# Kernel tuning notes

Hardware: AMD Instinct MI355X
Metric: run time of the kernel (lower is better)

Reference implementation:

```python
import jax, jax.numpy as jnp
import numpy as np

T = 32768       # sequence length (batch=1 in original forward)
DY = 63         # mark dim; input_size = DY + 1 = 64
D_IN = 64
H = 256         # hidden_size
OUT = 32        # out_size
NI = 1024       # number of inducing points


def _lstm_scan(x, w_ih, w_hh, b_ih, b_hh, reverse):
    """Single-direction LSTM over [T, D] input, batch=1. PyTorch gate order i,f,g,o."""
    xg = x @ w_ih.T + (b_ih + b_hh)  # [T, 4H], input projection precomputed

    def step(carry, xg_t):
        h, c = carry
        g = xg_t + h @ w_hh.T
        i, f, gg, o = jnp.split(g, 4)
        c = jax.nn.sigmoid(f) * c + jax.nn.sigmoid(i) * jnp.tanh(gg)
        h = jax.nn.sigmoid(o) * jnp.tanh(c)
        return (h, c), h

    init = (jnp.zeros((H,), x.dtype), jnp.zeros((H,), x.dtype))
    _, hs = jax.lax.scan(step, init, xg, reverse=reverse)
    return hs  # [T, H]


def _bilstm(x, layer_params):
    for (wf, uf, bif, bhf, wb, ub, bib, bhb) in layer_params:
        hf = _lstm_scan(x, wf, uf, bif, bhf, False)
        hb = _lstm_scan(x, wb, ub, bib, bhb, True)
        x = jnp.concatenate([hf, hb], axis=-1)  # [T, 2H]
    return x


def setup_inputs() -> dict:
    key = jax.random.key(0)
    ks = iter(jax.random.split(key, 24))
    s = 1.0 / np.sqrt(H)  # PyTorch LSTM uniform(-1/sqrt(H), 1/sqrt(H)) init
    def U(shape):
        return jax.random.uniform(next(ks), shape, jnp.float32, -s, s)
    inp = {
        "Y": jax.random.normal(next(ks), (T, DY), jnp.float32),
        "dT": jax.random.uniform(next(ks), (T,), jnp.float32),
        "induce_idx": jnp.sort(jax.random.randint(next(ks), (NI,), 0, T)),
        # layer 0: input D_IN; layer 1: input 2H (bidirectional)
        "w_ih_l0f": U((4 * H, D_IN)), "w_hh_l0f": U((4 * H, H)), "b_ih_l0f": U((4 * H,)), "b_hh_l0f": U((4 * H,)),
        "w_ih_l0b": U((4 * H, D_IN)), "w_hh_l0b": U((4 * H, H)), "b_ih_l0b": U((4 * H,)), "b_hh_l0b": U((4 * H,)),
        "w_ih_l1f": U((4 * H, 2 * H)), "w_hh_l1f": U((4 * H, H)), "b_ih_l1f": U((4 * H,)), "b_hh_l1f": U((4 * H,)),
        "w_ih_l1b": U((4 * H, 2 * H)), "w_hh_l1b": U((4 * H, H)), "b_ih_l1b": U((4 * H,)), "b_hh_l1b": U((4 * H,)),
        "fc_weight": jax.random.normal(next(ks), (2 * H, 2 * OUT), jnp.float32),
    }
    return inp


def reference(Y, dT, induce_idx,
              w_ih_l0f, w_hh_l0f, b_ih_l0f, b_hh_l0f,
              w_ih_l0b, w_hh_l0b, b_ih_l0b, b_hh_l0b,
              w_ih_l1f, w_hh_l1f, b_ih_l1f, b_hh_l1f,
              w_ih_l1b, w_hh_l1b, b_ih_l1b, b_hh_l1b,
              fc_weight):
    x = jnp.concatenate([Y, dT[:, None]], axis=1)  # [T, D_IN]
    layer_params = [
        (w_ih_l0f, w_hh_l0f, b_ih_l0f, b_hh_l0f, w_ih_l0b, w_hh_l0b, b_ih_l0b, b_hh_l0b),
        (w_ih_l1f, w_hh_l1f, b_ih_l1f, b_hh_l1f, w_ih_l1b, w_hh_l1b, b_ih_l1b, b_hh_l1b),
    ]
    h = _bilstm(x, layer_params)          # [T, 2H]
    out = h @ fc_weight                    # [T, 2*OUT]
    sel = out[induce_idx]                  # [NI, 2*OUT]
    return sel[:, :OUT], sel[:, OUT:]
```

## Files before the change

### kernel.cpp

```cpp
#include <hip/hip_runtime.h>

typedef unsigned int u32;
typedef unsigned short u16;
typedef _Float16 f16;
typedef _Float16 f16x2 __attribute__((ext_vector_type(2)));
typedef _Float16 f16x4 __attribute__((ext_vector_type(4)));

#define T_SEQ 32768

static const size_t OFF_DT   = 0;
static const size_t OFF_FLG  = 1024;
static const size_t OFF_MAP  = 4096;
static const size_t OFF_H1G  = 135168;
static const size_t OFF_BIAS = 1183744;
static const size_t OFF_FCW  = 1200128;
static const size_t OFF_WQ8  = 1331200;
static const size_t OFF_WIH0 = 3428352;
static const size_t OFF_WIH1 = 3690496;
static const size_t OFF_XQ   = 5787648;
static const size_t OFF_H0   = 9981952;
static const size_t OFF_XG   = 43536384;
static const size_t XG_DIR   = (size_t)T_SEQ * 1024 * 2;
static const size_t NEED_PAR = OFF_XG + 2 * XG_DIR;

__device__ __forceinline__ float bf2f(u16 u) {
  union { u32 i; float f; } v; v.i = ((u32)u) << 16; return v.f;
}
__device__ __forceinline__ u16 f2bf(float f) {
  union { float f; u32 i; } v; v.f = f;
  u32 u = v.i;
  return (u16)((u + 0x7fffu + ((u >> 16) & 1u)) >> 16);
}
__device__ __forceinline__ u32 packf2(float a, float b) {
  f16x2 p; p.x = (f16)a; p.y = (f16)b;
  return __builtin_bit_cast(u32, p);
}
__device__ __forceinline__ u32 bf2f2(u32 v) {
  union { u32 i; float f; } lo, hi;
  lo.i = v << 16; hi.i = v & 0xffff0000u;
  return packf2(lo.f, hi.f);
}
__device__ __forceinline__ float ldf(const void* p, size_t i, u32 isf) {
  return isf ? ((const float*)p)[i] : bf2f(((const u16*)p)[i]);
}
__device__ __forceinline__ float fdot2f(f16x2 a, f16x2 b, float c) {
#if __has_builtin(__builtin_amdgcn_fdot2)
  return __builtin_amdgcn_fdot2(a, b, c, false);
#else
  return c + (float)a.x * (float)b.x + (float)a.y * (float)b.y;
#endif
}
__device__ __forceinline__ float fdotu(u32 a, u32 b, float c) {
  return fdot2f(__builtin_bit_cast(f16x2, a), __builtin_bit_cast(f16x2, b), c);
}
__device__ __forceinline__ int sdot4(u32 a, u32 b, int c) {
#if __has_builtin(__builtin_amdgcn_sdot4)
  return __builtin_amdgcn_sdot4((int)a, (int)b, c, false);
#else
  int r = c;
#pragma unroll
  for (int j = 0; j < 4; ++j)
    r += (int)(signed char)(a >> (8 * j)) * (int)(signed char)(b >> (8 * j));
  return r;
#endif
}
__device__ __forceinline__ int dpp_xor1(int x) {
#if __has_builtin(__builtin_amdgcn_update_dpp)
  return __builtin_amdgcn_update_dpp(0, x, 0xB1, 0xF, 0xF, true);
#else
  return __shfl_xor(x, 1);
#endif
}
__device__ __forceinline__ int dpp_xor2(int x) {
#if __has_builtin(__builtin_amdgcn_update_dpp)
  return __builtin_amdgcn_update_dpp(0, x, 0x4E, 0xF, 0xF, true);
#else
  return __shfl_xor(x, 2);
#endif
}
__device__ __forceinline__ int dpp_ror8(int x) {
#if __has_builtin(__builtin_amdgcn_update_dpp)
  return __builtin_amdgcn_update_dpp(0, x, 0x128, 0xF, 0xF, true);
#else
  return __shfl_xor(x, 8);
#endif
}
__device__ __forceinline__ int swz_xor4(int x) {
#if __has_builtin(__builtin_amdgcn_ds_swizzle)
  return __builtin_amdgcn_ds_swizzle(x, 0x101F);
#else
  return __shfl_xor(x, 4);
#endif
}
template <int CTRL>
__device__ __forceinline__ float dpp_bcastf(float x) {
#if __has_builtin(__builtin_amdgcn_update_dpp)
  return __builtin_bit_cast(float,
      __builtin_amdgcn_update_dpp(0, __builtin_bit_cast(int, x), CTRL, 0xF, 0xF, true));
#else
  return __shfl(x, (threadIdx.x & ~3) + (CTRL & 3));
#endif
}
__device__ __forceinline__ float tanhf_fast(float x) {
  return 1.0f - 2.0f * __builtin_amdgcn_rcpf(1.0f + __builtin_amdgcn_exp2f(2.8853900817779268f * x));
}
__device__ __forceinline__ void wg_barrier_lds() {
  asm volatile("s_waitcnt lgkmcnt(0)" ::: "memory");
  __builtin_amdgcn_s_barrier();
  asm volatile("" ::: "memory");
}

__global__ void k_detect(const u16* __restrict__ probe, u32* __restrict__ dt) {
  __shared__ int cnt;
  if (threadIdx.x == 0) cnt = 0;
  __syncthreads();
  int bad = 0;
  for (int i = threadIdx.x; i < 8192; i += 256) {
    float v = bf2f(probe[i]);
    if (!(v * v <= 16.0f)) bad++;
  }
  atomicAdd(&cnt, bad);
  __syncthreads();
  if (threadIdx.x == 0) *dt = (cnt > 64) ? 1u : 0u;
}

__global__ void k_conv_pairs(const void* __restrict__ src, u32* __restrict__ dst,
                             int np, const u32* __restrict__ dtp) {
  u32 isf = *dtp;
  int i = blockIdx.x * 256 + threadIdx.x;
  if (i >= np) return;
  if (isf) {
    const float* s = (const float*)src;
    dst[i] = packf2(s[2 * i], s[2 * i + 1]);
  } else {
    dst[i] = bf2f2(((const u32*)src)[i]);
  }
}

__global__ void k_quant(const void* __restrict__ src, u32* __restrict__ dst,
                        const u32* __restrict__ dtp) {
  u32 isf = *dtp;
  int i = blockIdx.x * 256 + threadIdx.x;
  int row = i >> 6, c = i & 63;
  u32 out = 0;
#pragma unroll
  for (int j = 0; j < 4; ++j) {
    float w = ldf(src, (size_t)row * 256 + 4 * c + j, isf);
    int q = (int)rintf(w * 2048.0f);
    q = q > 127 ? 127 : (q < -127 ? -127 : q);
    out |= ((u32)(q & 0xff)) << (8 * j);
  }
  dst[i] = out;
}

__global__ void k_conv_misc(const void* bi0f, const void* bh0f, const void* bi0b, const void* bh0b,
                            const void* bi1f, const void* bh1f, const void* bi1b, const void* bh1b,
                            const void* fcb, float* __restrict__ bias, float* __restrict__ fcw,
                            u32* __restrict__ flags, int* __restrict__ map,
                            const u32* __restrict__ dtp) {
  u32 isf = *dtp;
  int i = blockIdx.x * 256 + threadIdx.x;
  if (i < 4096) {
    int ld = i >> 10, r = i & 1023;
    const void* bi; const void* bh;
    if (ld == 0)      { bi = bi0f; bh = bh0f; }
    else if (ld == 1) { bi = bi0b; bh = bh0b; }
    else if (ld == 2) { bi = bi1f; bh = bh1f; }
    else              { bi = bi1b; bh = bh1b; }
    bias[i] = ldf(bi, r, isf) + ldf(bh, r, isf);
  } else if (i < 36864) {
    fcw[i - 4096] = ldf(fcb, i - 4096, isf);
  } else if (i < 36992) {
    flags[i - 36864] = 0;
  } else if (i < 69760) {
    map[i - 36992] = -1;
  }
}

__global__ void k_conv_x(const void* __restrict__ Y, const void* __restrict__ dT,
                         u32* __restrict__ xq, const u32* __restrict__ dtp) {
  u32 isf = *dtp;
  int i = blockIdx.x * 256 + threadIdx.x;
  if (i >= T_SEQ * 32) return;
  int t = i >> 5, m = i & 31, k2 = 2 * m;
  float a = ldf(Y, (size_t)t * 63 + k2, isf);
  float b = (k2 + 1 < 63) ? ldf(Y, (size_t)t * 63 + k2 + 1, isf) : ldf(dT, t, isf);
  xq[i] = packf2(a, b);
}

__global__ void k_map_set(const int* __restrict__ idx, int* __restrict__ map) {
  int i = blockIdx.x * 256 + threadIdx.x;
  if (i < 1024) map[idx[i]] = i;
}

__global__ __launch_bounds__(256) void k_gemm(
    const u32* __restrict__ Aq, const u32* __restrict__ Wc,
    const float* __restrict__ bias, f16* __restrict__ xgT, int Kp, int rev) {
  int t0 = blockIdx.x << 6, r0 = blockIdx.y << 6;
  int tid = threadIdx.x, tx = tid & 15, ty = tid >> 4;
  __shared__ u32 As[64][33];
  __shared__ u32 Bs[64][33];
  float acc[4][4] = {};
  for (int kp0 = 0; kp0 < Kp; kp0 += 32) {
#pragma unroll
    for (int i = 0; i < 8; ++i) {
      int idx = tid + (i << 8);
      int row = idx >> 5, kp = idx & 31, kpg = kp0 + kp;
      As[row][kp] = Aq[(size_t)(t0 + row) * Kp + kpg];
      Bs[row][kp] = Wc[(size_t)(r0 + row) * Kp + kpg];
    }
    __syncthreads();
#pragma unroll 4
    for (int kk = 0; kk < 32; ++kk) {
      u32 av[4], bv[4];
#pragma unroll
      for (int i = 0; i < 4; ++i) av[i] = As[ty * 4 + i][kk];
#pragma unroll
      for (int i = 0; i < 4; ++i) bv[i] = Bs[tx * 4 + i][kk];
#pragma unroll
      for (int i = 0; i < 4; ++i)
#pragma unroll
        for (int j = 0; j < 4; ++j)
          acc[i][j] = fdotu(av[i], bv[j], acc[i][j]);
    }
    __syncthreads();
  }
  int tb = t0 + (ty << 2);
#pragma unroll
  for (int j = 0; j < 4; ++j) {
    int rr = r0 + tx * 4 + j;
    float b = bias[rr];
    f16 v0 = (f16)(acc[0][j] + b);
    f16 v1 = (f16)(acc[1][j] + b);
    f16 v2 = (f16)(acc[2][j] + b);
    f16 v3 = (f16)(acc[3][j] + b);
    size_t base = (size_t)rr * T_SEQ;
    f16x4 v;
    size_t pos;
    if (rev) { pos = base + (size_t)(T_SEQ - 4 - tb); v = (f16x4){v3, v2, v1, v0}; }
    else     { pos = base + (size_t)tb;               v = (f16x4){v0, v1, v2, v3}; }
    *(f16x4*)(xgT + pos) = v;
  }
}

template <bool HASMAP>
__global__ __launch_bounds__(1024)
__attribute__((amdgpu_waves_per_eu(4, 4))) void k_recur2(
    const f16* __restrict__ xgT, const u32* __restrict__ wq,
    f16* __restrict__ h_full, f16* __restrict__ h1g,
    const int* __restrict__ map, int dir0) {
  const int dir = dir0 + blockIdx.x;
  const int tid = threadIdx.x;
  const int g16 = tid >> 4;
  const int s = tid & 15;
  const int u = (g16 << 2) + (s >> 2);
  const u32* wqd = wq + ((size_t)dir << 16);

  __shared__ __align__(16) unsigned char hb8[2][256];

  uint4 w[16];
  {
    const uint4* pw = (const uint4*)wqd;
#pragma unroll
    for (int t = 0; t < 16; ++t) {
      int r = t ^ s;
      w[t] = pw[(size_t)((((r & 3) << 8) + (g16 << 2) + (r >> 2)) * 16 + s)];
    }
  }

  if (tid < 128) ((u32*)hb8)[tid] = 0;

  const float ksc = 1.0f / (2048.0f * 127.0f);
  const float sk = ((s & 3) == 2) ? 2.8853900817779268f : -1.4426950408889634f;
  const float aa = ((s & 3) == 2) ? -2.0f : 1.0f;
  const float bb = ((s & 3) == 2) ? 1.0f : 0.0f;

  const f16* xg_d = xgT + (size_t)blockIdx.x * ((size_t)T_SEQ * 1024);
  const f16* xrow = xg_d + (size_t)(((s & 3) << 8) | u) * T_SEQ;

  const int tstep = dir ? -1 : 1;
  int t = dir ? (T_SEQ - 1) : 0;
  int mp = HASMAP ? map[t] : -1;
  float c_state = 0.f;

  f16* hout = h_full ? (h_full + (size_t)t * 512 + (dir << 8) + u) : nullptr;
  const ptrdiff_t hstride = (ptrdiff_t)tstep * 512;

  uint4 xcur = *(const uint4*)xrow;
  uint4 xnxt = xcur;

  __syncthreads();

  for (int ch = 0; ch < T_SEQ / 8; ++ch) {
    if (ch + 1 < T_SEQ / 8) xnxt = *(const uint4*)(xrow + (((size_t)ch + 1) << 3));
#pragma unroll
    for (int j = 0; j < 8; ++j) {
      u32 dw = (j >> 1) == 0 ? xcur.x : (j >> 1) == 1 ? xcur.y
             : (j >> 1) == 2 ? xcur.z : xcur.w;
      f16x2 pr = __builtin_bit_cast(f16x2, dw);
      float xb = (float)((j & 1) ? pr.y : pr.x);

      int ms = mp;
      if (HASMAP) {
        int tn = t + tstep;
        int idx2 = ((unsigned)tn < T_SEQ) ? tn : t;
        mp = map[idx2];
      }

      uint4 hv = ((const uint4*)hb8)[((j & 1) << 4) + s];

      int a0, a1, a2, a3, a4, a5, a6, a7, a8, a9, a10, a11, a12, a13, a14, a15;
#define DOTSLOT(A, T)                                             \
      A = sdot4(w[T].w, hv.w,                                     \
          sdot4(w[T].z, hv.z,                                     \
          sdot4(w[T].y, hv.y,                                     \
          sdot4(w[T].x, hv.x, 0))));
      DOTSLOT(a0, 0)   DOTSLOT(a1, 1)   DOTSLOT(a2, 2)   DOTSLOT(a3, 3)
      DOTSLOT(a4, 4)   DOTSLOT(a5, 5)   DOTSLOT(a6, 6)   DOTSLOT(a7, 7)
      DOTSLOT(a8, 8)   DOTSLOT(a9, 9)   DOTSLOT(a10, 10) DOTSLOT(a11, 11)
      DOTSLOT(a12, 12) DOTSLOT(a13, 13) DOTSLOT(a14, 14) DOTSLOT(a15, 15)
#undef DOTSLOT
      int b0 = a0 + dpp_xor1(a1);
      int b1 = a2 + dpp_xor1(a3);
      int b2 = a4 + dpp_xor1(a5);
      int b3 = a6 + dpp_xor1(a7);
      int b4 = a8 + dpp_xor1(a9);
      int b5 = a10 + dpp_xor1(a11);
      int b6 = a12 + dpp_xor1(a13);
      int b7 = a14 + dpp_xor1(a15);
      int c0 = b0 + dpp_xor2(b1);
      int c1 = b2 + dpp_xor2(b3);
      int c2 = b4 + dpp_xor2(b5);
      int c3 = b6 + dpp_xor2(b7);
      int d0 = c0 + swz_xor4(c1);
      int d1 = c2 + swz_xor4(c3);
      int e  = d0 + dpp_ror8(d1);

      float x = __builtin_fmaf((float)e, ksc, xb);
      float r = __builtin_amdgcn_rcpf(1.0f + __builtin_amdgcn_exp2f(sk * x));
      float g = __builtin_fmaf(aa, r, bb);
      float gi = dpp_bcastf<0x00>(g);
      float gf = dpp_bcastf<0x55>(g);
      float gg = dpp_bcastf<0xAA>(g);
      float go = dpp_bcastf<0xFF>(g);
      c_state = __builtin_fmaf(gf, c_state, gi * gg);
      float h = go * tanhf_fast(c_state);
      int q8 = (int)rintf(h * 127.0f);
      if ((s & 3) == 0) {
        hb8[(j & 1) ^ 1][u] = (unsigned char)(q8 & 0xff);
        if (h_full) *hout = (f16)h;
        if (HASMAP && ms >= 0) h1g[(size_t)ms * 512 + (dir << 8) + u] = (f16)h;
      }
      wg_barrier_lds();
      t += tstep;
      hout += hstride;
    }
    xcur = xnxt;
  }
}

__global__ void k_fc(const f16* __restrict__ hbase, const int* __restrict__ mapn,
                     const int* __restrict__ idx, const float* __restrict__ fcw,
                     void* __restrict__ out, const u32* __restrict__ dtp) {
  u32 isf = *dtp;
  int n = blockIdx.x;
  int cc = threadIdx.x;
  int slot = mapn ? mapn[idx[n]] : idx[n];
  const f16* hp = hbase + (size_t)slot * 512;
  float acc = 0.f;
#pragma unroll 8
  for (int k = 0; k < 512; ++k) acc += (float)hp[k] * fcw[k * 64 + cc];
  int o = (cc < 32) ? (n * 32 + cc) : (32 * 1024 + n * 32 + (cc - 32));
  if (isf) ((float*)out)[o] = acc;
  else     ((u16*)out)[o]   = f2bf(acc);
}

extern "C" void kernel_launch(void* const* d_in, const int* in_sizes, int n_in,
                              void* d_out, int out_size, void* d_ws, size_t ws_size,
                              hipStream_t stream) {
  const void* Y        = d_in[0];
  const void* dT       = d_in[1];
  const int*  idx      = (const int*)d_in[2];
  const void* w_ih_l0f = d_in[3];
  const void* w_hh_l0f = d_in[4];
  const void* b_ih_l0f = d_in[5];
  const void* b_hh_l0f = d_in[6];
  const void* w_ih_l0b = d_in[7];
  const void* w_hh_l0b = d_in[8];
  const void* b_ih_l0b = d_in[9];
  const void* b_hh_l0b = d_in[10];
  const void* w_ih_l1f = d_in[11];
  const void* w_hh_l1f = d_in[12];
  const void* b_ih_l1f = d_in[13];
  const void* b_hh_l1f = d_in[14];
  const void* w_ih_l1b = d_in[15];
  const void* w_hh_l1b = d_in[16];
  const void* b_ih_l1b = d_in[17];
  const void* b_hh_l1b = d_in[18];
  const void* fcbf     = d_in[19];

  char* ws = (char*)d_ws;
  u32*  dt    = (u32*)(ws + OFF_DT);
  u32*  flags = (u32*)(ws + OFF_FLG);
  int*  map   = (int*)(ws + OFF_MAP);
  f16*  h1g   = (f16*)(ws + OFF_H1G);
  float* bias = (float*)(ws + OFF_BIAS);
  float* fcw  = (float*)(ws + OFF_FCW);
  u32*  wq8   = (u32*)(ws + OFF_WQ8);
  u32*  wih0  = (u32*)(ws + OFF_WIH0);
  u32*  wih1  = (u32*)(ws + OFF_WIH1);
  u32*  xq    = (u32*)(ws + OFF_XQ);
  f16*  h0    = (f16*)(ws + OFF_H0);
  f16*  xg    = (f16*)(ws + OFF_XG);
  f16*  xg1   = xg + XG_DIR / 2;

  const int par = (ws_size >= NEED_PAR) ? 1 : 0;

  k_detect<<<1, 256, 0, stream>>>((const u16*)w_hh_l0f, dt);
  k_quant<<<256, 256, 0, stream>>>(w_hh_l0f, wq8 + 0 * 65536, dt);
  k_quant<<<256, 256, 0, stream>>>(w_hh_l0b, wq8 + 1 * 65536, dt);
  k_quant<<<256, 256, 0, stream>>>(w_hh_l1f, wq8 + 2 * 65536, dt);
  k_quant<<<256, 256, 0, stream>>>(w_hh_l1b, wq8 + 3 * 65536, dt);
  k_conv_pairs<<<128, 256, 0, stream>>>(w_ih_l0f, wih0 + 0, 32768, dt);
  k_conv_pairs<<<128, 256, 0, stream>>>(w_ih_l0b, wih0 + 32768, 32768, dt);
  k_conv_pairs<<<1024, 256, 0, stream>>>(w_ih_l1f, wih1 + 0, 262144, dt);
  k_conv_pairs<<<1024, 256, 0, stream>>>(w_ih_l1b, wih1 + 262144, 262144, dt);
  k_conv_misc<<<273, 256, 0, stream>>>(b_ih_l0f, b_hh_l0f, b_ih_l0b, b_hh_l0b,
                                       b_ih_l1f, b_hh_l1f, b_ih_l1b, b_hh_l1b,
                                       fcbf, bias, fcw, flags, map, dt);
  k_conv_x<<<4096, 256, 0, stream>>>(Y, dT, xq, dt);
  k_map_set<<<4, 256, 0, stream>>>(idx, map);

  dim3 ggrid(T_SEQ / 64, 16);
  if (par) {
    k_gemm<<<ggrid, 256, 0, stream>>>(xq, wih0, bias, xg, 32, 0);
    k_gemm<<<ggrid, 256, 0, stream>>>(xq, wih0 + 32768, bias + 1024, xg1, 32, 1);
    k_recur2<false><<<2, 1024, 0, stream>>>(xg, wq8, h0, nullptr, nullptr, 0);
    k_gemm<<<ggrid, 256, 0, stream>>>((const u32*)h0, wih1, bias + 2048, xg, 256, 0);
    k_gemm<<<ggrid, 256, 0, stream>>>((const u32*)h0, wih1 + 262144, bias + 3072, xg1, 256, 1);
    k_recur2<false><<<2, 1024, 0, stream>>>(xg, wq8 + 2 * 65536, h0, nullptr, nullptr, 0);
    k_fc<<<1024, 64, 0, stream>>>(h0, nullptr, idx, fcw, d_out, dt);
  } else {
    k_gemm<<<ggrid, 256, 0, stream>>>(xq, wih0, bias, xg, 32, 0);
    k_recur2<false><<<1, 1024, 0, stream>>>(xg, wq8, h0, nullptr, nullptr, 0);
    k_gemm<<<ggrid, 256, 0, stream>>>(xq, wih0 + 32768, bias + 1024, xg, 32, 1);
    k_recur2<false><<<1, 1024, 0, stream>>>(xg, wq8, h0, nullptr, nullptr, 1);
    k_gemm<<<ggrid, 256, 0, stream>>>((const u32*)h0, wih1, bias + 2048, xg, 256, 0);
    k_recur2<true><<<1, 1024, 0, stream>>>(xg, wq8 + 2 * 65536, nullptr, h1g, map, 0);
    k_gemm<<<ggrid, 256, 0, stream>>>((const u32*)h0, wih1 + 262144, bias + 3072, xg, 256, 1);
    k_recur2<true><<<1, 1024, 0, stream>>>(xg, wq8 + 2 * 65536, nullptr, h1g, map, 1);
    k_fc<<<1024, 64, 0, stream>>>(h1g, map, idx, fcw, d_out, dt);
  }
}
```

Before: 61.59 ms.

## Remap LSTM recurrence lanes to 8-lane groups with doubled per-lane dot width

Reorganizes the thread-to-work mapping in the recurrent kernel so each lane handles 32-byte slices of the hidden vector across 8 weight slots. This removes the ds_swizzle cross-lane reduction stage and half of the DPP adds, shortening the per-timestep critical path. It also folds the sigmoid scale constant into the fma so one multiply is dropped. The cost is two LDS vector reads per lane per step instead of one, plus a more complex weight layout at load time.

```diff
diff --git a/kernel.cpp b/kernel.cpp
--- a/kernel.cpp
+++ b/kernel.cpp
@@ -83,13 +83,6 @@
   return __builtin_amdgcn_update_dpp(0, x, 0x128, 0xF, 0xF, true);
 #else
   return __shfl_xor(x, 8);
-#endif
-}
-__device__ __forceinline__ int swz_xor4(int x) {
-#if __has_builtin(__builtin_amdgcn_ds_swizzle)
-  return __builtin_amdgcn_ds_swizzle(x, 0x101F);
-#else
-  return __shfl_xor(x, 4);
 #endif
 }
 template <int CTRL>
@@ -244,16 +237,17 @@
 }
 
 template <bool HASMAP>
-__global__ __launch_bounds__(1024)
-__attribute__((amdgpu_waves_per_eu(4, 4))) void k_recur2(
+__global__ __launch_bounds__(1024, 4) void k_recur2(
     const f16* __restrict__ xgT, const u32* __restrict__ wq,
     f16* __restrict__ h_full, f16* __restrict__ h1g,
     const int* __restrict__ map, int dir0) {
   const int dir = dir0 + blockIdx.x;
   const int tid = threadIdx.x;
-  const int g16 = tid >> 4;
-  const int s = tid & 15;
-  const int u = (g16 << 2) + (s >> 2);
+  const int l = tid & 63, wv = tid >> 6;
+  const int r16 = l >> 4, gbit = (l >> 2) & 1;
+  const int s = (l & 3) | ((l >> 1) & 4);
+  const int ubase = (wv << 4) + (r16 << 2) + (gbit << 1);
+  const int u_own = ubase + (s >> 2);
   const u32* wqd = wq + ((size_t)dir << 16);
 
   __shared__ __align__(16) unsigned char hb8[2][256];
@@ -262,9 +256,11 @@
   {
     const uint4* pw = (const uint4*)wqd;
 #pragma unroll
-    for (int t = 0; t < 16; ++t) {
-      int r = t ^ s;
-      w[t] = pw[(size_t)((((r & 3) << 8) + (g16 << 2) + (r >> 2)) * 16 + s)];
+    for (int t = 0; t < 8; ++t) {
+      int rho = t ^ s;
+      int R = ((rho & 3) << 8) | (ubase + (rho >> 2));
+      w[2 * t]     = pw[(size_t)R * 16 + 2 * s];
+      w[2 * t + 1] = pw[(size_t)R * 16 + 2 * s + 1];
     }
   }
 
@@ -274,16 +270,17 @@
   const float sk = ((s & 3) == 2) ? 2.8853900817779268f : -1.4426950408889634f;
   const float aa = ((s & 3) == 2) ? -2.0f : 1.0f;
   const float bb = ((s & 3) == 2) ? 1.0f : 0.0f;
+  const float kk = sk * ksc;
 
   const f16* xg_d = xgT + (size_t)blockIdx.x * ((size_t)T_SEQ * 1024);
-  const f16* xrow = xg_d + (size_t)(((s & 3) << 8) | u) * T_SEQ;
+  const f16* xrow = xg_d + (size_t)(((s & 3) << 8) | u_own) * T_SEQ;
 
   const int tstep = dir ? -1 : 1;
   int t = dir ? (T_SEQ - 1) : 0;
   int mp = HASMAP ? map[t] : -1;
   float c_state = 0.f;
 
-  f16* hout = h_full ? (h_full + (size_t)t * 512 + (dir << 8) + u) : nullptr;
+  f16* hout = h_full ? (h_full + (size_t)t * 512 + (dir << 8) + u_own) : nullptr;
   const ptrdiff_t hstride = (ptrdiff_t)tstep * 512;
 
   uint4 xcur = *(const uint4*)xrow;
@@ -298,7 +295,7 @@
       u32 dw = (j >> 1) == 0 ? xcur.x : (j >> 1) == 1 ? xcur.y
              : (j >> 1) == 2 ? xcur.z : xcur.w;
       f16x2 pr = __builtin_bit_cast(f16x2, dw);
-      float xb = (float)((j & 1) ? pr.y : pr.x);
+      float xbs = sk * (float)((j & 1) ? pr.y : pr.x);
 
       int ms = mp;
       if (HASMAP) {
@@ -307,37 +304,32 @@
         mp = map[idx2];
       }
 
-      uint4 hv = ((const uint4*)hb8)[((j & 1) << 4) + s];
-
-      int a0, a1, a2, a3, a4, a5, a6, a7, a8, a9, a10, a11, a12, a13, a14, a15;
+      const uint4* hp = (const uint4*)hb8 + ((j & 1) << 4) + (s << 1);
+      uint4 hv0 = hp[0], hv1 = hp[1];
+
+      int a0, a1, a2, a3, a4, a5, a6, a7;
 #define DOTSLOT(A, T)                                             \
-      A = sdot4(w[T].w, hv.w,                                     \
-          sdot4(w[T].z, hv.z,                                     \
-          sdot4(w[T].y, hv.y,                                     \
-          sdot4(w[T].x, hv.x, 0))));
-      DOTSLOT(a0, 0)   DOTSLOT(a1, 1)   DOTSLOT(a2, 2)   DOTSLOT(a3, 3)
-      DOTSLOT(a4, 4)   DOTSLOT(a5, 5)   DOTSLOT(a6, 6)   DOTSLOT(a7, 7)
-      DOTSLOT(a8, 8)   DOTSLOT(a9, 9)   DOTSLOT(a10, 10) DOTSLOT(a11, 11)
-      DOTSLOT(a12, 12) DOTSLOT(a13, 13) DOTSLOT(a14, 14) DOTSLOT(a15, 15)
+      A = sdot4(w[2*T+1].w, hv1.w,                                \
+          sdot4(w[2*T+1].z, hv1.z,                                \
+          sdot4(w[2*T+1].y, hv1.y,                                \
+          sdot4(w[2*T+1].x, hv1.x,                                \
+          sdot4(w[2*T].w,   hv0.w,                                \
+          sdot4(w[2*T].z,   hv0.z,                                \
+          sdot4(w[2*T].y,   hv0.y,                                \
+          sdot4(w[2*T].x,   hv0.x, 0))))))));
+      DOTSLOT(a0, 0) DOTSLOT(a1, 1) DOTSLOT(a2, 2) DOTSLOT(a3, 3)
+      DOTSLOT(a4, 4) DOTSLOT(a5, 5) DOTSLOT(a6, 6) DOTSLOT(a7, 7)
 #undef DOTSLOT
       int b0 = a0 + dpp_xor1(a1);
       int b1 = a2 + dpp_xor1(a3);
       int b2 = a4 + dpp_xor1(a5);
       int b3 = a6 + dpp_xor1(a7);
-      int b4 = a8 + dpp_xor1(a9);
-      int b5 = a10 + dpp_xor1(a11);
-      int b6 = a12 + dpp_xor1(a13);
-      int b7 = a14 + dpp_xor1(a15);
       int c0 = b0 + dpp_xor2(b1);
       int c1 = b2 + dpp_xor2(b3);
-      int c2 = b4 + dpp_xor2(b5);
-      int c3 = b6 + dpp_xor2(b7);
-      int d0 = c0 + swz_xor4(c1);
-      int d1 = c2 + swz_xor4(c3);
-      int e  = d0 + dpp_ror8(d1);
-
-      float x = __builtin_fmaf((float)e, ksc, xb);
-      float r = __builtin_amdgcn_rcpf(1.0f + __builtin_amdgcn_exp2f(sk * x));
+      int e  = c0 + dpp_ror8(c1);
+
+      float xarg = __builtin_fmaf((float)e, kk, xbs);
+      float r = __builtin_amdgcn_rcpf(1.0f + __builtin_amdgcn_exp2f(xarg));
       float g = __builtin_fmaf(aa, r, bb);
       float gi = dpp_bcastf<0x00>(g);
       float gf = dpp_bcastf<0x55>(g);
@@ -346,10 +338,10 @@
       c_state = __builtin_fmaf(gf, c_state, gi * gg);
       float h = go * tanhf_fast(c_state);
       int q8 = (int)rintf(h * 127.0f);
-      if ((s & 3) == 0) {
-        hb8[(j & 1) ^ 1][u] = (unsigned char)(q8 & 0xff);
+      if ((l & 3) == 0) {
+        hb8[(j & 1) ^ 1][u_own] = (unsigned char)(q8 & 0xff);
         if (h_full) *hout = (f16)h;
-        if (HASMAP && ms >= 0) h1g[(size_t)ms * 512 + (dir << 8) + u] = (f16)h;
+        if (HASMAP && ms >= 0) h1g[(size_t)ms * 512 + (dir << 8) + u_own] = (f16)h;
       }
       wg_barrier_lds();
       t += tstep;
```

Measured after the change: 61.07 ms. No clear change (-0.8%).
